# Kernel tuning notes

Measured on AMD Instinct MI355X. Metric: run time of the kernel, lower is better.

## Reference

```python
import jax, jax.numpy as jnp
import numpy as np

N = 1024
H = 128


def setup_inputs() -> dict:
    key = jax.random.key(0)
    k1, k2, k3, k4, k5, k6 = jax.random.split(key, 6)
    s = 1.0 / np.sqrt(H)
    return {
        "node_feats": jax.random.normal(k1, (N, H), dtype=jnp.float32),
        "edge_attr": jax.random.normal(k2, (N * N, H), dtype=jnp.float32),
        "We": jax.random.uniform(k3, (H, H), jnp.float32, -s, s),
        "be": jax.random.uniform(k4, (H,), jnp.float32, -s, s),
        "Wi": jax.random.uniform(k5, (H, H), jnp.float32, -s, s),
        "Wj": jax.random.uniform(k6, (H, H), jnp.float32, -s, s),
    }


def reference(node_feats, edge_attr, We, be, Wi, Wj):
    # f_ij: [N^2, H] linear with bias
    f_ij = edge_attr @ We.T + be
    # f_i, f_j: [N, H] linears without bias
    f_i = node_feats @ Wi.T
    f_j = node_feats @ Wj.T
    # torch.matmul on 1-D vectors -> scalar dot; broadcast into each H-wide row.
    dots = jnp.einsum("ih,jh->ij", f_i, f_j)  # [N, N]
    fi_fj = dots.reshape(-1, 1)                 # [N^2, 1], broadcasts over H
    return jax.nn.relu(f_ij + fi_fj)
```

## Files before the change

kernel.cpp:

```cpp
#include <hip/hip_runtime.h>
#include <hip/hip_bf16.h>
#include <stdint.h>
#include <stddef.h>

typedef __bf16 bf16_t;
typedef __bf16 bf16x8 __attribute__((ext_vector_type(8)));
typedef float  f32x4  __attribute__((ext_vector_type(4)));

#define NN 1024
#define H  128
#define GRID 8192

__global__ void k_cvt_we(const float* __restrict__ src, bf16_t* __restrict__ dst) {
    int i = blockIdx.x * 256 + threadIdx.x;
    if (i < H * H) dst[i] = (bf16_t)src[i];
}

__global__ void k_proj(const float* __restrict__ node,
                       const float* __restrict__ Wi,
                       const float* __restrict__ Wj,
                       bf16_t* __restrict__ fi,
                       bf16_t* __restrict__ fj) {
    __shared__ float nrow[H];
    const int row = blockIdx.x;
    const int t   = threadIdx.x;
    const int h   = t & (H - 1);
    const int sel = t >> 7;
    if (t < H) nrow[t] = node[(size_t)row * H + t];
    __syncthreads();
    const float* w = (sel ? Wj : Wi) + (size_t)h * H;
    float acc = 0.f;
    #pragma unroll
    for (int k4 = 0; k4 < H / 4; ++k4) {
        f32x4 wv = *(const f32x4*)(w + k4 * 4);
        f32x4 nv = *(const f32x4*)(&nrow[k4 * 4]);
        acc += nv[0] * wv[0] + nv[1] * wv[1] + nv[2] * wv[2] + nv[3] * wv[3];
    }
    bf16_t* dst = sel ? fj : fi;
    dst[(size_t)row * H + h] = (bf16_t)acc;
}

__global__ __launch_bounds__(256, 4)
void k_dots(const bf16_t* __restrict__ fi,
            const bf16_t* __restrict__ fj,
            float* __restrict__ dots) {
    const int t    = threadIdx.x;
    const int wave = t >> 6;
    const int lane = t & 63;
    const int l15  = lane & 15;
    const int g    = lane >> 4;

    const int bm    = blockIdx.x >> 3;
    const int bn    = blockIdx.x & 7;
    const int ibase = bm * 128 + wave * 32;
    const int jbase = bn * 128;

    f32x4 acc[2][8];
    #pragma unroll
    for (int mf = 0; mf < 2; ++mf)
        #pragma unroll
        for (int nt = 0; nt < 8; ++nt)
            acc[mf][nt] = (f32x4){0.f, 0.f, 0.f, 0.f};

    const bf16_t* a0 = fi + (size_t)(ibase +  0 + l15) * H + g * 8;
    const bf16_t* a1 = fi + (size_t)(ibase + 16 + l15) * H + g * 8;

    #pragma unroll
    for (int kst = 0; kst < 4; ++kst) {
        bf16x8 af0 = *(const bf16x8*)(a0 + kst * 32);
        bf16x8 af1 = *(const bf16x8*)(a1 + kst * 32);
        #pragma unroll
        for (int nt = 0; nt < 8; ++nt) {
            bf16x8 bf = *(const bf16x8*)(fj + (size_t)(jbase + nt * 16 + l15) * H + kst * 32 + g * 8);
            acc[0][nt] = __builtin_amdgcn_mfma_f32_16x16x32_bf16(af0, bf, acc[0][nt], 0, 0, 0);
            acc[1][nt] = __builtin_amdgcn_mfma_f32_16x16x32_bf16(af1, bf, acc[1][nt], 0, 0, 0);
        }
    }

    #pragma unroll
    for (int mf = 0; mf < 2; ++mf) {
        const int rbase = ibase + mf * 16 + g * 4;
        #pragma unroll
        for (int r = 0; r < 4; ++r) {
            #pragma unroll
            for (int nt = 0; nt < 8; ++nt)
                dots[(size_t)(rbase + r) * NN + jbase + nt * 16 + l15] = acc[mf][nt][r];
        }
    }
}

__device__ __forceinline__ void gl_lds16(const float* g, float* l) {
    __builtin_amdgcn_global_load_lds(
        (const __attribute__((address_space(1))) unsigned int*)g,
        (__attribute__((address_space(3))) unsigned int*)l,
        16, 0, 0);
}

__global__ __launch_bounds__(64, 2)
void k_main(const float* __restrict__ edge,
            const bf16_t* __restrict__ web,
            const float* __restrict__ be,
            const float* __restrict__ dots,
            float* __restrict__ out) {
    __shared__ __align__(16) float buf[3][16][H];

    const int lane  = threadIdx.x;
    const int l15   = lane & 15;
    const int g     = lane >> 4;
    const int lhalf = lane >> 5;
    const int b16   = (lane & 31) * 16;

    bf16x8 wfr[8][4];
    {
        const bf16_t* wp = web + (size_t)l15 * H + g * 8;
        #pragma unroll
        for (int nt = 0; nt < 8; ++nt)
            #pragma unroll
            for (int kk = 0; kk < 4; ++kk)
                wfr[nt][kk] = *(const bf16x8*)(wp + (size_t)(nt * 16) * H + kk * 32);
    }
    f32x4 bvv[8];
    #pragma unroll
    for (int nt = 0; nt < 8; ++nt)
        bvv[nt] = *(const f32x4*)(be + nt * 16 + g * 4);

    float dvv[8];
    #pragma unroll
    for (int k = 0; k < 8; ++k)
        dvv[k] = dots[(size_t)(blockIdx.x + k * GRID) * 16 + l15];

    #pragma unroll
    for (int nt = 0; nt < 8; ++nt) {
        #pragma unroll
        for (int kk = 0; kk < 4; ++kk)
            asm volatile("" : "+v"(wfr[nt][kk]));
        asm volatile("" : "+v"(bvv[nt]));
        asm volatile("" : "+v"(dvv[nt]));
    }

    #define STAGE(K, BI)                                                         \
        {                                                                        \
            const char* tb = (const char*)(edge + (size_t)(blockIdx.x + (K) * GRID) * 16 * H); \
            _Pragma("unroll")                                                    \
            for (int i = 0; i < 8; ++i) {                                        \
                const int r = 2 * i + lhalf;                                     \
                const int srcoff = r * 512 + (b16 ^ ((r & 7) << 4));             \
                gl_lds16((const float*)(tb + srcoff), &buf[BI][2 * i][0]);       \
            }                                                                    \
        }

    STAGE(0, 0)
    STAGE(1, 1)

    const int sw = (l15 & 7) << 4;

    #pragma unroll
    for (int k = 0; k < 8; ++k) {
        if (k == 0)                 asm volatile("s_waitcnt vmcnt(8)"  ::: "memory");
        else if (k == 1 || k == 7)  asm volatile("s_waitcnt vmcnt(16)" ::: "memory");
        else                        asm volatile("s_waitcnt vmcnt(24)" ::: "memory");
        __builtin_amdgcn_sched_barrier(0);

        if (k < 6) STAGE(k + 2, (k + 2) % 3)

        const float dv = dvv[k];
        f32x4 acc[8];
        #pragma unroll
        for (int nt = 0; nt < 8; ++nt) {
            #pragma unroll
            for (int r = 0; r < 4; ++r) acc[nt][r] = bvv[nt][r] + dv;
        }

        const char* lrow = (const char*)&buf[k % 3][0][0] + l15 * 512;
        #pragma unroll
        for (int kk = 0; kk < 4; ++kk) {
            f32x4 u0 = *(const f32x4*)(lrow + kk * 128 + ((g * 32 +  0) ^ sw));
            f32x4 u1 = *(const f32x4*)(lrow + kk * 128 + ((g * 32 + 16) ^ sw));
            bf16x8 bfrag;
            #pragma unroll
            for (int i2 = 0; i2 < 4; ++i2) {
                bfrag[i2]     = (bf16_t)u0[i2];
                bfrag[i2 + 4] = (bf16_t)u1[i2];
            }
            #pragma unroll
            for (int nt = 0; nt < 8; ++nt)
                acc[nt] = __builtin_amdgcn_mfma_f32_16x16x32_bf16(wfr[nt][kk], bfrag, acc[nt], 0, 0, 0);
        }

        float* op = out + ((size_t)(blockIdx.x + k * GRID) * 16 + l15) * H + g * 4;
        #pragma unroll
        for (int nt = 0; nt < 8; ++nt) {
            f32x4 v;
            #pragma unroll
            for (int r = 0; r < 4; ++r) v[r] = fmaxf(acc[nt][r], 0.f);
            *(f32x4*)(op + nt * 16) = v;
        }
    }
    #undef STAGE
}

extern "C" void kernel_launch(void* const* d_in, const int* in_sizes, int n_in,
                              void* d_out, int out_size, void* d_ws, size_t ws_size,
                              hipStream_t stream) {
    const float* node = (const float*)d_in[0];
    const float* edge = (const float*)d_in[1];
    const float* We   = (const float*)d_in[2];
    const float* be   = (const float*)d_in[3];
    const float* Wi   = (const float*)d_in[4];
    const float* Wj   = (const float*)d_in[5];
    float* out = (float*)d_out;

    char* w = (char*)d_ws;
    bf16_t* fi_bf = (bf16_t*)w;
    bf16_t* fj_bf = (bf16_t*)(w + (256 << 10));
    float*  dots  = (float*)(w + (512 << 10));
    bf16_t* web   = (bf16_t*)(w + (512 << 10) + (4 << 20));

    k_cvt_we<<<(H * H + 255) / 256, 256, 0, stream>>>(We, web);
    k_proj<<<NN, 256, 0, stream>>>(node, Wi, Wj, fi_bf, fj_bf);
    k_dots<<<64, 256, 0, stream>>>(fi_bf, fj_bf, dots);
    k_main<<<GRID, 64, 0, stream>>>(edge, web, be, dots, out);
}
```

Before: 257.1 us.

## Use 4-wave blocks with double-buffered LDS staging in main kernel

```diff
diff --git a/kernel.cpp b/kernel.cpp
--- a/kernel.cpp
+++ b/kernel.cpp
@@ -9,7 +9,7 @@
 
 #define NN 1024
 #define H  128
-#define GRID 8192
+#define GRID 2048
 
 __global__ void k_cvt_we(const float* __restrict__ src, bf16_t* __restrict__ dst) {
     int i = blockIdx.x * 256 + threadIdx.x;
@@ -52,41 +52,31 @@
 
     const int bm    = blockIdx.x >> 3;
     const int bn    = blockIdx.x & 7;
-    const int ibase = bm * 128 + wave * 32;
+    const int ibase = bm * 64 + wave * 16;
     const int jbase = bn * 128;
 
-    f32x4 acc[2][8];
-    #pragma unroll
-    for (int mf = 0; mf < 2; ++mf)
-        #pragma unroll
-        for (int nt = 0; nt < 8; ++nt)
-            acc[mf][nt] = (f32x4){0.f, 0.f, 0.f, 0.f};
-
-    const bf16_t* a0 = fi + (size_t)(ibase +  0 + l15) * H + g * 8;
-    const bf16_t* a1 = fi + (size_t)(ibase + 16 + l15) * H + g * 8;
+    f32x4 acc[8];
+    #pragma unroll
+    for (int nt = 0; nt < 8; ++nt) acc[nt] = (f32x4){0.f, 0.f, 0.f, 0.f};
+
+    const bf16_t* a = fi + (size_t)(ibase + l15) * H + g * 8;
 
     #pragma unroll
     for (int kst = 0; kst < 4; ++kst) {
-        bf16x8 af0 = *(const bf16x8*)(a0 + kst * 32);
-        bf16x8 af1 = *(const bf16x8*)(a1 + kst * 32);
+        bf16x8 af = *(const bf16x8*)(a + kst * 32);
         #pragma unroll
         for (int nt = 0; nt < 8; ++nt) {
             bf16x8 bf = *(const bf16x8*)(fj + (size_t)(jbase + nt * 16 + l15) * H + kst * 32 + g * 8);
-            acc[0][nt] = __builtin_amdgcn_mfma_f32_16x16x32_bf16(af0, bf, acc[0][nt], 0, 0, 0);
-            acc[1][nt] = __builtin_amdgcn_mfma_f32_16x16x32_bf16(af1, bf, acc[1][nt], 0, 0, 0);
-        }
-    }
-
-    #pragma unroll
-    for (int mf = 0; mf < 2; ++mf) {
-        const int rbase = ibase + mf * 16 + g * 4;
-        #pragma unroll
-        for (int r = 0; r < 4; ++r) {
-            #pragma unroll
-            for (int nt = 0; nt < 8; ++nt)
-                dots[(size_t)(rbase + r) * NN + jbase + nt * 16 + l15] = acc[mf][nt][r];
-        }
-    }
+            acc[nt] = __builtin_amdgcn_mfma_f32_16x16x32_bf16(af, bf, acc[nt], 0, 0, 0);
+        }
+    }
+
+    const int rbase = ibase + g * 4;
+    #pragma unroll
+    for (int r = 0; r < 4; ++r)
+        #pragma unroll
+        for (int nt = 0; nt < 8; ++nt)
+            dots[(size_t)(rbase + r) * NN + jbase + nt * 16 + l15] = acc[nt][r];
 }
 
 __device__ __forceinline__ void gl_lds16(const float* g, float* l) {
@@ -96,20 +86,27 @@
         16, 0, 0);
 }
 
-__global__ __launch_bounds__(64, 2)
+__global__ __launch_bounds__(256, 2)
 void k_main(const float* __restrict__ edge,
             const bf16_t* __restrict__ web,
             const float* __restrict__ be,
             const float* __restrict__ dots,
             float* __restrict__ out) {
-    __shared__ __align__(16) float buf[3][16][H];
-
-    const int lane  = threadIdx.x;
+    __shared__ __align__(16) float bufA[64][H];
+    __shared__ __align__(16) float bufB[64][H];
+    __shared__ float lbias[H];
+
+    const int t     = threadIdx.x;
+    const int wave  = t >> 6;
+    const int lane  = t & 63;
     const int l15   = lane & 15;
     const int g     = lane >> 4;
     const int lhalf = lane >> 5;
     const int b16   = (lane & 31) * 16;
 
+    if (t < H) lbias[t] = be[t];
+    __syncthreads();
+
     bf16x8 wfr[8][4];
     {
         const bf16_t* wp = web + (size_t)l15 * H + g * 8;
@@ -119,75 +116,77 @@
             for (int kk = 0; kk < 4; ++kk)
                 wfr[nt][kk] = *(const bf16x8*)(wp + (size_t)(nt * 16) * H + kk * 32);
     }
-    f32x4 bvv[8];
-    #pragma unroll
-    for (int nt = 0; nt < 8; ++nt)
-        bvv[nt] = *(const f32x4*)(be + nt * 16 + g * 4);
-
     float dvv[8];
     #pragma unroll
     for (int k = 0; k < 8; ++k)
-        dvv[k] = dots[(size_t)(blockIdx.x + k * GRID) * 16 + l15];
+        dvv[k] = dots[(size_t)(blockIdx.x + k * GRID) * 64 + wave * 16 + l15];
 
     #pragma unroll
     for (int nt = 0; nt < 8; ++nt) {
         #pragma unroll
         for (int kk = 0; kk < 4; ++kk)
             asm volatile("" : "+v"(wfr[nt][kk]));
-        asm volatile("" : "+v"(bvv[nt]));
         asm volatile("" : "+v"(dvv[nt]));
     }
 
-    #define STAGE(K, BI)                                                         \
+    #define STAGE(K, BUFP)                                                       \
         {                                                                        \
-            const char* tb = (const char*)(edge + (size_t)(blockIdx.x + (K) * GRID) * 16 * H); \
+            const char* tb = (const char*)(edge + ((size_t)(blockIdx.x + (K) * GRID) * 64 + wave * 16) * H); \
             _Pragma("unroll")                                                    \
             for (int i = 0; i < 8; ++i) {                                        \
                 const int r = 2 * i + lhalf;                                     \
                 const int srcoff = r * 512 + (b16 ^ ((r & 7) << 4));             \
-                gl_lds16((const float*)(tb + srcoff), &buf[BI][2 * i][0]);       \
+                gl_lds16((const float*)(tb + srcoff), &BUFP[wave * 16 + 2 * i][0]); \
             }                                                                    \
         }
 
-    STAGE(0, 0)
-    STAGE(1, 1)
+    STAGE(0, bufA)
 
     const int sw = (l15 & 7) << 4;
 
     #pragma unroll
     for (int k = 0; k < 8; ++k) {
-        if (k == 0)                 asm volatile("s_waitcnt vmcnt(8)"  ::: "memory");
-        else if (k == 1 || k == 7)  asm volatile("s_waitcnt vmcnt(16)" ::: "memory");
-        else                        asm volatile("s_waitcnt vmcnt(24)" ::: "memory");
+        if (k == 0) asm volatile("s_waitcnt vmcnt(0)" ::: "memory");
+        else        asm volatile("s_waitcnt vmcnt(8)" ::: "memory");
         __builtin_amdgcn_sched_barrier(0);
 
-        if (k < 6) STAGE(k + 2, (k + 2) % 3)
+        const char* lrow = (const char*)((k & 1) ? &bufB[0][0] : &bufA[0][0])
+                         + (wave * 16 + l15) * 512;
+        f32x4 u[8];
+        #pragma unroll
+        for (int kk = 0; kk < 4; ++kk) {
+            u[2 * kk]     = *(const f32x4*)(lrow + kk * 128 + ((g * 32 +  0) ^ sw));
+            u[2 * kk + 1] = *(const f32x4*)(lrow + kk * 128 + ((g * 32 + 16) ^ sw));
+        }
+
+        if (k < 7) {
+            if (k & 1) { STAGE(k + 1, bufA) }
+            else       { STAGE(k + 1, bufB) }
+        }
 
         const float dv = dvv[k];
         f32x4 acc[8];
         #pragma unroll
         for (int nt = 0; nt < 8; ++nt) {
-            #pragma unroll
-            for (int r = 0; r < 4; ++r) acc[nt][r] = bvv[nt][r] + dv;
-        }
-
-        const char* lrow = (const char*)&buf[k % 3][0][0] + l15 * 512;
+            f32x4 bv = *(const f32x4*)(&lbias[nt * 16 + g * 4]);
+            #pragma unroll
+            for (int r = 0; r < 4; ++r) acc[nt][r] = bv[r] + dv;
+        }
+
         #pragma unroll
         for (int kk = 0; kk < 4; ++kk) {
-            f32x4 u0 = *(const f32x4*)(lrow + kk * 128 + ((g * 32 +  0) ^ sw));
-            f32x4 u1 = *(const f32x4*)(lrow + kk * 128 + ((g * 32 + 16) ^ sw));
             bf16x8 bfrag;
             #pragma unroll
             for (int i2 = 0; i2 < 4; ++i2) {
-                bfrag[i2]     = (bf16_t)u0[i2];
-                bfrag[i2 + 4] = (bf16_t)u1[i2];
+                bfrag[i2]     = (bf16_t)u[2 * kk][i2];
+                bfrag[i2 + 4] = (bf16_t)u[2 * kk + 1][i2];
             }
             #pragma unroll
             for (int nt = 0; nt < 8; ++nt)
                 acc[nt] = __builtin_amdgcn_mfma_f32_16x16x32_bf16(wfr[nt][kk], bfrag, acc[nt], 0, 0, 0);
         }
 
-        float* op = out + ((size_t)(blockIdx.x + k * GRID) * 16 + l15) * H + g * 4;
+        float* op = out + ((size_t)(blockIdx.x + k * GRID) * 64 + wave * 16 + l15) * H + g * 4;
         #pragma unroll
         for (int nt = 0; nt < 8; ++nt) {
             f32x4 v;
@@ -218,6 +217,6 @@
 
     k_cvt_we<<<(H * H + 255) / 256, 256, 0, stream>>>(We, web);
     k_proj<<<NN, 256, 0, stream>>>(node, Wi, Wj, fi_bf, fj_bf);
-    k_dots<<<64, 256, 0, stream>>>(fi_bf, fj_bf, dots);
-    k_main<<<GRID, 64, 0, stream>>>(edge, web, be, dots, out);
-}
+    k_dots<<<128, 256, 0, stream>>>(fi_bf, fj_bf, dots);
+    k_main<<<GRID, 256, 0, stream>>>(edge, web, be, dots, out);
+}
```

New measurement: 244.9 us. 4.7% less time.
